# Kernel tuning notes

Measured on AMD Instinct MI355X. Metric: run time of the kernel, lower is better.

Reference implementation:

```python
import jax, jax.numpy as jnp
import numpy as np

MAX_CLUSTERS = 5
CLUSTER_SIZE_MAX = 3
K_HOP = 2
TAU = 1.0  # epoch=0 -> tau_init * decay^0 = 1.0
NEG = -1e9


def _logits(x, ctx, W1, b1, W2, b2):
    # x: [B,N,D], ctx: [B,H] -> logits [B,N] (selection_mlp, dropout=eval/identity)
    B, N, _ = x.shape
    h = jnp.concatenate([x, jnp.broadcast_to(ctx[:, None, :], (B, N, ctx.shape[-1]))], axis=-1)
    h = jax.nn.relu(h @ W1.T + b1)
    return (h @ W2.T + b2)[..., 0]


def _select(logits, cand, key):
    # Hard Gumbel-Softmax argmax over candidate nodes; zeros row if no candidates.
    any_c = cand.any(axis=-1, keepdims=True)
    ml = jnp.where(cand, logits, NEG)
    u = jax.random.uniform(key, logits.shape, dtype=logits.dtype)
    g = -jnp.log(-jnp.log(u + 1e-8) + 1e-8)
    idx = jnp.argmax((ml + g) / TAU, axis=-1)
    oh = jax.nn.one_hot(idx, logits.shape[-1], dtype=logits.dtype)
    return oh * any_c.astype(logits.dtype)


def _gru(seq, h0, Wih, Whh, bih, bhh):
    # torch nn.GRU single layer, batch_first; seq: [B,T,D], h0: [B,H] -> final hidden [B,H]
    def cell(h, xt):
        gi = xt @ Wih.T + bih
        gh = h @ Whh.T + bhh
        ir, iz, inn = jnp.split(gi, 3, axis=-1)
        hr, hz, hn = jnp.split(gh, 3, axis=-1)
        r = jax.nn.sigmoid(ir + hr)
        z = jax.nn.sigmoid(iz + hz)
        n = jnp.tanh(inn + r * hn)
        return (1.0 - z) * n + z * h, None
    h, _ = jax.lax.scan(cell, h0, jnp.swapaxes(seq, 0, 1))
    return h


def reference(x, adj, mask, W1, b1, W2, b2, Wc, bc, Wih, Whh, bih, bhh):
    B, N, D = x.shape
    key = jax.random.key(42)
    avail = mask.astype(bool)
    ctx = x.mean(axis=1) @ Wc.T + bc          # context_init  [B,H]
    h_gru = jnp.zeros_like(ctx)               # context_hidden
    assign = jnp.zeros((B, N, MAX_CLUSTERS), x.dtype)
    embs, hist = [], []
    for c in range(MAX_CLUSTERS):
        # logits are identical for every selection within this cluster (same x, same context)
        logits = _logits(x, ctx, W1, b1, W2, b2)  # [B,N]
        # seed selection (torch uses .item() -> selection is a constant index; no grad path)
        seed = jax.lax.stop_gradient(_select(logits, avail, jax.random.fold_in(key, 2 * c)))
        avail = avail & ~(seed > 0.5)
        # k-hop BFS from seed via adjacency matvecs
        reach = seed > 0.5
        cur = seed
        for _ in range(K_HOP):
            nb = jnp.einsum('bn,bnm->bm', cur, adj) > 0
            new = nb & ~reach
            reach = reach | nb
            cur = new.astype(x.dtype)
        member = seed
        for a in range(CLUSTER_SIZE_MAX - 1):
            cand = avail & reach
            sel = jax.lax.stop_gradient(_select(logits, cand, jax.random.fold_in(key, 2 * c + 1000 + a)))
            avail = avail & ~(sel > 0.5)
            member = member + sel
        assign = assign.at[:, :, c].set(member)
        cnt = member.sum(axis=-1, keepdims=True)
        emb = jnp.einsum('bn,bnd->bd', member, x) / jnp.maximum(cnt, 1.0)  # mean of member feats; 0 if empty
        embs.append(emb)
        hist.append(emb)
        # torch re-runs the GRU over the FULL cluster history each iteration, starting
        # from the previously updated hidden state (faithful to the original code)
        h_gru = _gru(jnp.stack(hist, axis=1), h_gru, Wih, Whh, bih, bhh)
        ctx = h_gru
    cluster_features = jnp.stack(embs, axis=1)               # [B,S,D]
    S = MAX_CLUSTERS
    cluster_adj = jnp.ones((B, S, S), x.dtype) - jnp.eye(S, dtype=x.dtype)[None]
    return cluster_features, cluster_adj, assign


def setup_inputs() -> dict:
    key = jax.random.key(0)
    ks = jax.random.split(key, 10)
    B, N, D, H = 16, 2048, 128, 64
    x = jax.random.normal(ks[0], (B, N, D), dtype=jnp.float32)
    # sparse symmetric binary adjacency, ~16 neighbors per node
    a = (jax.random.uniform(ks[1], (B, N, N)) < 0.004).astype(jnp.float32)
    adj = jnp.clip(a + jnp.swapaxes(a, 1, 2), 0.0, 1.0)
    adj = adj * (1.0 - jnp.eye(N, dtype=jnp.float32)[None])
    mask = jnp.ones((B, N), dtype=jnp.int32)
    s = 0.05
    return {
        'x': x, 'adj': adj, 'mask': mask,
        'W1': jax.random.normal(ks[2], (H, D + H)) * s, 'b1': jnp.zeros((H,)),
        'W2': jax.random.normal(ks[3], (1, H)) * s, 'b2': jnp.zeros((1,)),
        'Wc': jax.random.normal(ks[4], (H, D)) * s, 'bc': jnp.zeros((H,)),
        'Wih': jax.random.normal(ks[5], (3 * H, D)) * s,
        'Whh': jax.random.normal(ks[6], (3 * H, H)) * s,
        'bih': jnp.zeros((3 * H,)), 'bhh': jnp.zeros((3 * H,)),
    }
```

## Files before the change

### kernel.cpp

```cpp
#include <hip/hip_runtime.h>
#include <cfloat>
#include <cmath>

#define NB 2048
#define BB 16
#define DD 128
#define HH 64
#define MAXC 5
#define CSMAX 3
#define NT 1024

__device__ __forceinline__ unsigned rotl32(unsigned v, int d) {
  return (v << d) | (v >> (32 - d));
}

__device__ __forceinline__ void tf2x32(unsigned k0, unsigned k1, unsigned x0, unsigned x1,
                                       unsigned& o0, unsigned& o1) {
  unsigned ks2 = k0 ^ k1 ^ 0x1BD11BDAu;
  x0 += k0; x1 += k1;
#define RND(r) { x0 += x1; x1 = rotl32(x1, r); x1 ^= x0; }
  RND(13) RND(15) RND(26) RND(6)   x0 += k1;  x1 += ks2 + 1u;
  RND(17) RND(29) RND(16) RND(24)  x0 += ks2; x1 += k0 + 2u;
  RND(13) RND(15) RND(26) RND(6)   x0 += k0;  x1 += k1 + 3u;
  RND(17) RND(29) RND(16) RND(24)  x0 += k1;  x1 += ks2 + 4u;
  RND(13) RND(15) RND(26) RND(6)   x0 += ks2; x1 += k0 + 5u;
#undef RND
  o0 = x0; o1 = x1;
}

__device__ __forceinline__ float gumbel_for(unsigned k0, unsigned k1, unsigned idx) {
  unsigned o0, o1;
  tf2x32(k0, k1, 0u, idx, o0, o1);
  unsigned bits = o0 ^ o1;
  float u = __uint_as_float((bits >> 9) | 0x3f800000u) - 1.0f;
  float uu = u + 1e-8f;
  return -logf(-logf(uu) + 1e-8f);
}

__global__ __launch_bounds__(NT) void gvp_prep(
    const float* __restrict__ x, const float* __restrict__ W1,
    float* __restrict__ P, float* __restrict__ partial, float* __restrict__ gumb) {
  __shared__ __align__(16) float s_W1[HH][DD + 4];
  __shared__ float sp[8][DD];
  const int bid = blockIdx.x, tid = threadIdx.x;

  if (bid < 128) {
    for (int i = tid; i < HH * (DD / 4); i += NT) {
      int r = i >> 5, q = i & 31;
      *(float4*)&s_W1[r][q * 4] = *(const float4*)(W1 + (size_t)r * (DD + HH) + q * 4);
    }
    __syncthreads();
    const int jg = tid & 15, ng = tid >> 4;
    const int j0 = jg * 4;
    const size_t n0 = (size_t)bid * 256 + ng * 4;
    const float4* x4 = (const float4*)x;
    float acc[4][4];
#pragma unroll
    for (int i = 0; i < 4; i++)
#pragma unroll
      for (int q = 0; q < 4; q++) acc[i][q] = 0.f;
    for (int kq = 0; kq < 32; kq++) {
      float4 xv[4], wv[4];
#pragma unroll
      for (int i = 0; i < 4; i++) xv[i] = x4[(n0 + i) * 32 + kq];
#pragma unroll
      for (int q = 0; q < 4; q++) wv[q] = *(const float4*)&s_W1[j0 + q][kq * 4];
#pragma unroll
      for (int i = 0; i < 4; i++)
#pragma unroll
        for (int q = 0; q < 4; q++)
          acc[i][q] += xv[i].x * wv[q].x + xv[i].y * wv[q].y +
                       xv[i].z * wv[q].z + xv[i].w * wv[q].w;
    }
#pragma unroll
    for (int i = 0; i < 4; i++)
#pragma unroll
      for (int q = 0; q < 4; q++)
        P[(n0 + i) * HH + j0 + q] = acc[i][q];
  } else if (bid < 384) {
    const int bm = bid - 128;
    const int b = bm >> 4, chunk = bm & 15;
    const int d = tid & (DD - 1), part = tid >> 7;
    float acc = 0.f;
    const int base = chunk * 128 + part;
#pragma unroll
    for (int k = 0; k < 16; k++)
      acc += x[((size_t)b * NB + base + k * 8) * DD + d];
    sp[part][d] = acc;
    __syncthreads();
    if (tid < DD) {
      float m = 0.f;
#pragma unroll
      for (int p = 0; p < 8; p++) m += sp[p][tid];
      partial[((size_t)b * 16 + chunk) * DD + tid] = m;
    }
  } else {
    const int bg = bid - 384;
    const int base = (bg * NT + tid) * 4;
#pragma unroll
    for (int i = 0; i < 4; i++) {
      int idx = base + i;
      int sel = idx >> 15;
      int rem = idx & 32767;
      int c = sel / 3, s = sel - 3 * c;
      unsigned data = (s == 0) ? (unsigned)(2 * c) : (unsigned)(2 * c + 1000 + (s - 1));
      unsigned k0, k1;
      tf2x32(0u, 42u, 0u, data, k0, k1);
      gumb[idx] = gumbel_for(k0, k1, (unsigned)rem);
    }
  }
}

__global__ __launch_bounds__(NT, 4) void gvp_main(
    const float* __restrict__ x, const float* __restrict__ adj, const int* __restrict__ mask,
    const float* __restrict__ W1, const float* __restrict__ b1,
    const float* __restrict__ W2, const float* __restrict__ b2,
    const float* __restrict__ Wc, const float* __restrict__ bc,
    const float* __restrict__ Wih, const float* __restrict__ Whh,
    const float* __restrict__ bih, const float* __restrict__ bhh,
    const float* __restrict__ P, const float* __restrict__ partial,
    const float* __restrict__ gumb,
    float* __restrict__ out_feat, float* __restrict__ out_adjm, float* __restrict__ out_assign) {
  const int b = blockIdx.x;
  const int tid = threadIdx.x;

  __shared__ __align__(16) float s_logits[NB];
  __shared__ __align__(16) float s_gumb[2][NB];
  __shared__ unsigned char s_avail[NB], s_reach[NB], s_assignB[NB];
  __shared__ short s_list[128];
  __shared__ int s_cnt;
  __shared__ unsigned long long s_key[CSMAX];
  __shared__ __align__(16) float s_ctx[HH], s_q[HH];
  __shared__ __align__(16) float s_h[2][HH];
  __shared__ __align__(16) float s_hist[MAXC][DD];
  __shared__ __align__(16) float s_giAll[MAXC][3 * HH];
  __shared__ __align__(16) float s_Whh[3 * HH][HH + 4];
  __shared__ __align__(16) float s_W1c[HH][HH + 4];
  __shared__ __align__(16) float s_W2[HH];
  __shared__ float s_bhh[3 * HH], s_b1[HH];
  __shared__ __align__(16) float s_mean[DD];
  __shared__ float s_b2v;

  const size_t xb = (size_t)b * NB * DD;
  const float4* adj4 = (const float4*)(adj + (size_t)b * NB * NB);
  const float4* P4 = (const float4*)(P + (size_t)b * NB * HH);
  const int n0 = tid, n1 = tid + NT;

  auto scanReduce = [&](float bv, int bi, int slot) {
#pragma unroll
    for (int off = 32; off; off >>= 1) {
      float ov = __shfl_down(bv, off);
      int oi = __shfl_down(bi, off);
      if (ov > bv || (ov == bv && oi < bi)) { bv = ov; bi = oi; }
    }
    if ((tid & 63) == 0 && bi < NB) {
      unsigned u = __float_as_uint(bv);
      u = (u & 0x80000000u) ? ~u : (u | 0x80000000u);
      unsigned long long key = ((unsigned long long)u << 32) | (unsigned)(~bi);
      atomicMax(&s_key[slot], key);
    }
  };
  auto decodeIdx = [](unsigned long long k) -> int {
    return k ? (int)(unsigned)(~(unsigned)k) : -1;
  };

  float4 pP[16];
  {
    const float4* pr0 = P4 + (size_t)n0 * 16;
#pragma unroll
    for (int i = 0; i < 16; i++) pP[i] = pr0[i];
  }
  for (int i = tid; i < 3 * HH * (HH / 4); i += NT) {
    int r = i >> 4, q = i & 15;
    *(float4*)&s_Whh[r][q * 4] = *(const float4*)(Whh + (size_t)r * HH + q * 4);
  }
  {
    int r = tid >> 4, q = tid & 15;
    *(float4*)&s_W1c[r][q * 4] = *(const float4*)(W1 + (size_t)r * (DD + HH) + DD + q * 4);
  }
  if (tid < 3 * HH) s_bhh[tid] = bhh[tid];
  if (tid < HH) { s_W2[tid] = W2[tid]; s_b1[tid] = b1[tid]; s_h[0][tid] = 0.f; }
  if (tid == 0) s_b2v = b2[0];
#pragma unroll
  for (int r = 0; r < 2; r++) {
    int n = tid + r * NT;
    s_avail[n] = (mask[b * NB + n] != 0) ? 1 : 0;
    s_assignB[n] = 0;
  }
  if (tid < DD) {
    float m = 0.f;
#pragma unroll
    for (int k = 0; k < 16; k++) m += partial[((size_t)b * 16 + k) * DD + tid];
    s_mean[tid] = m * (1.0f / NB);
  }
  float4 gst;
  float g0a, g0b;
  {
    const float* g0p = gumb + ((size_t)0 * BB + b) * NB;
    g0a = g0p[n0]; g0b = g0p[n1];
    const float4* g12 = (const float4*)(gumb + ((size_t)(1 + (tid >> 9)) * BB + b) * NB);
    gst = g12[tid & 511];
  }
  __syncthreads();
  if (tid < 4 * HH) {
    int row = tid >> 2, g = tid & 3;
    const float4* wr = (const float4*)(Wc + (size_t)row * DD) + g * 8;
    const float4* m4 = (const float4*)s_mean + g * 8;
    float s = 0.f;
#pragma unroll
    for (int i = 0; i < 8; i++) {
      float4 w = wr[i], m = m4[i];
      s += w.x * m.x + w.y * m.y + w.z * m.z + w.w * m.w;
    }
    s += __shfl_xor(s, 1);
    s += __shfl_xor(s, 2);
    if (g == 0) s_ctx[row] = s + bc[row];
  }
  __syncthreads();

  int hp = 0;

  auto gruStep = [&](int t, int lo, int c) {
    int tt = tid - lo;
    if ((unsigned)tt < 256u) {
      int row = tt >> 2, g = tt & 3;
      const float4* h4 = (const float4*)s_h[hp] + g * 4;
      float4 hv[4];
#pragma unroll
      for (int i = 0; i < 4; i++) hv[i] = h4[i];
      const float4* wr = (const float4*)&s_Whh[row][0] + g * 4;
      const float4* wz = (const float4*)&s_Whh[HH + row][0] + g * 4;
      const float4* wn = (const float4*)&s_Whh[2 * HH + row][0] + g * 4;
      float sr = 0.f, sz = 0.f, sn = 0.f;
#pragma unroll
      for (int i = 0; i < 4; i++) {
        float4 a = wr[i], bz = wz[i], cn = wn[i], h = hv[i];
        sr += a.x * h.x + a.y * h.y + a.z * h.z + a.w * h.w;
        sz += bz.x * h.x + bz.y * h.y + bz.z * h.z + bz.w * h.w;
        sn += cn.x * h.x + cn.y * h.y + cn.z * h.z + cn.w * h.w;
      }
      sr += __shfl_xor(sr, 1); sr += __shfl_xor(sr, 2);
      sz += __shfl_xor(sz, 1); sz += __shfl_xor(sz, 2);
      sn += __shfl_xor(sn, 1); sn += __shfl_xor(sn, 2);
      if (g == 0) {
        float r = 1.f / (1.f + expf(-(s_giAll[t][row] + sr + s_bhh[row])));
        float z = 1.f / (1.f + expf(-(s_giAll[t][HH + row] + sz + s_bhh[HH + row])));
        float nn = tanhf(s_giAll[t][2 * HH + row] + r * (sn + s_bhh[2 * HH + row]));
        float hn = (1.f - z) * nn + z * s_h[hp][row];
        s_h[hp ^ 1][row] = hn;
        if (t == c) s_ctx[row] = hn;
      }
    }
  };

  for (int c = 0; c < MAXC; c++) {
    ((float4*)s_gumb)[tid] = gst;
    if (tid < 4 * HH) {
      int row = tid >> 2, g = tid & 3;
      const float4* wr = (const float4*)&s_W1c[row][0] + g * 4;
      const float4* c4 = (const float4*)s_ctx + g * 4;
      float s = 0.f;
#pragma unroll
      for (int i = 0; i < 4; i++) {
        float4 w = wr[i], cc = c4[i];
        s += w.x * cc.x + w.y * cc.y + w.z * cc.z + w.w * cc.w;
      }
      s += __shfl_xor(s, 1);
      s += __shfl_xor(s, 2);
      if (g == 0) s_q[row] = s + s_b1[row];
    }
    if (tid >= 512 && tid < 512 + CSMAX) s_key[tid - 512] = 0ull;
    if (tid == 768) s_cnt = 0;
    __syncthreads();

    {
      const float4* p1 = P4 + (size_t)n1 * 16;
      const float4* q4 = (const float4*)s_q;
      const float4* w4 = (const float4*)s_W2;
      float4 Pa[8];
#pragma unroll
      for (int i = 0; i < 8; i++) Pa[i] = p1[i];
      float l0 = s_b2v, l1 = s_b2v;
#pragma unroll
      for (int i = 0; i < 16; i++) {
        float4 p = pP[i], qv = q4[i], w = w4[i];
        l0 += w.x * fmaxf(p.x + qv.x, 0.f) + w.y * fmaxf(p.y + qv.y, 0.f) +
              w.z * fmaxf(p.z + qv.z, 0.f) + w.w * fmaxf(p.w + qv.w, 0.f);
      }
#pragma unroll
      for (int i = 0; i < 8; i++) {
        float4 p = Pa[i], qv = q4[i], w = w4[i];
        l1 += w.x * fmaxf(p.x + qv.x, 0.f) + w.y * fmaxf(p.y + qv.y, 0.f) +
              w.z * fmaxf(p.z + qv.z, 0.f) + w.w * fmaxf(p.w + qv.w, 0.f);
      }
#pragma unroll
      for (int i = 0; i < 8; i++) Pa[i] = p1[8 + i];
#pragma unroll
      for (int i = 0; i < 8; i++) {
        float4 p = Pa[i], qv = q4[8 + i], w = w4[8 + i];
        l1 += w.x * fmaxf(p.x + qv.x, 0.f) + w.y * fmaxf(p.y + qv.y, 0.f) +
              w.z * fmaxf(p.z + qv.z, 0.f) + w.w * fmaxf(p.w + qv.w, 0.f);
      }
      s_logits[n0] = l0;
      s_logits[n1] = l1;
      float bv = -FLT_MAX;
      int bi = NB;
      if (s_avail[n0]) { float y = l0 + g0a; if (y > bv) { bv = y; bi = n0; } }
      if (s_avail[n1]) { float y = l1 + g0b; if (y > bv || (y == bv && n1 < bi)) { bv = y; bi = n1; } }
      scanReduce(bv, bi, 0);
    }
    __syncthreads();

    const int seed = decodeIdx(s_key[0]);
    if (tid < 512) {
      if (seed >= 0) {
        float4 a = adj4[(size_t)seed * 512 + tid];
        int m = tid << 2;
        unsigned f0 = a.x > 0.f, f1 = a.y > 0.f, f2 = a.z > 0.f, f3 = a.w > 0.f;
        unsigned r = f0 | (f1 << 8) | (f2 << 16) | (f3 << 24);
        if ((seed >> 2) == tid) r |= 1u << ((seed & 3) * 8);
        ((unsigned*)s_reach)[tid] = r;
        if (f0 && m != seed)     { int p = atomicAdd(&s_cnt, 1); if (p < 128) s_list[p] = (short)m; }
        if (f1 && m + 1 != seed) { int p = atomicAdd(&s_cnt, 1); if (p < 128) s_list[p] = (short)(m + 1); }
        if (f2 && m + 2 != seed) { int p = atomicAdd(&s_cnt, 1); if (p < 128) s_list[p] = (short)(m + 2); }
        if (f3 && m + 3 != seed) { int p = atomicAdd(&s_cnt, 1); if (p < 128) s_list[p] = (short)(m + 3); }
      } else {
        ((unsigned*)s_reach)[tid] = 0u;
      }
    }
    __syncthreads();

    if (seed >= 0) {
      int cnt = min(s_cnt, 128);
      int m4 = tid & 511, rg = tid >> 9;
      bool a0 = false, a1 = false, a2 = false, a3 = false;
#pragma unroll
      for (int k = 0; k < 20; k++) {
        int li = rg + 2 * k;
        if (li < cnt) {
          int n = s_list[li];
          float4 a = adj4[(size_t)n * 512 + m4];
          a0 |= a.x > 0.f; a1 |= a.y > 0.f; a2 |= a.z > 0.f; a3 |= a.w > 0.f;
        }
      }
      for (int li = rg + 40; li < cnt; li += 2) {
        int n = s_list[li];
        float4 a = adj4[(size_t)n * 512 + m4];
        a0 |= a.x > 0.f; a1 |= a.y > 0.f; a2 |= a.z > 0.f; a3 |= a.w > 0.f;
      }
      int m = m4 << 2;
      if (a0) s_reach[m] = 1;
      if (a1) s_reach[m + 1] = 1;
      if (a2) s_reach[m + 2] = 1;
      if (a3) s_reach[m + 3] = 1;
    }
    __syncthreads();

    {
      float bv = -FLT_MAX;
      int bi = NB;
#pragma unroll
      for (int r = 0; r < 2; r++) {
        int n = tid + r * NT;
        if (s_avail[n] && s_reach[n] && n != seed) {
          float y = s_logits[n] + s_gumb[0][n];
          if (y > bv || (y == bv && n < bi)) { bv = y; bi = n; }
        }
      }
      scanReduce(bv, bi, 1);
    }
    __syncthreads();

    const int w1i = decodeIdx(s_key[1]);
    {
      float bv = -FLT_MAX;
      int bi = NB;
#pragma unroll
      for (int r = 0; r < 2; r++) {
        int n = tid + r * NT;
        if (s_avail[n] && s_reach[n] && n != seed && n != w1i) {
          float y = s_logits[n] + s_gumb[1][n];
          if (y > bv || (y == bv && n < bi)) { bv = y; bi = n; }
        }
      }
      scanReduce(bv, bi, 2);
    }
    __syncthreads();

    const int w2i = decodeIdx(s_key[2]);
    if (c + 1 < MAXC) {
      const float* g0p = gumb + ((size_t)((c + 1) * 3) * BB + b) * NB;
      g0a = g0p[n0]; g0b = g0p[n1];
      const float4* g12 =
          (const float4*)(gumb + ((size_t)((c + 1) * 3 + 1 + (tid >> 9)) * BB + b) * NB);
      gst = g12[tid & 511];
    }
    {
      int mc = (seed >= 0) + (w1i >= 0) + (w2i >= 0);
      if (tid < DD) {
        float acc = 0.f;
        if (seed >= 0) acc += x[xb + (size_t)seed * DD + tid];
        if (w1i >= 0) acc += x[xb + (size_t)w1i * DD + tid];
        if (w2i >= 0) acc += x[xb + (size_t)w2i * DD + tid];
        float e = acc / fmaxf((float)mc, 1.0f);
        s_hist[c][tid] = e;
        out_feat[((size_t)b * MAXC + c) * DD + tid] = e;
      } else if (tid >= 512 && tid < 512 + CSMAX) {
        int idx = (tid == 512) ? seed : (tid == 513 ? w1i : w2i);
        if (idx >= 0) { s_avail[idx] = 0; s_assignB[idx] |= (unsigned char)(1 << c); }
      }
      if (c >= 1) gruStep(0, 256, c);
    }
    __syncthreads();
    if (c >= 1) hp ^= 1;

    if (tid < 4 * 3 * HH) {
      int row = tid >> 2, g = tid & 3;
      const float4* wr = (const float4*)(Wih + (size_t)row * DD) + g * 8;
      const float4* h4 = (const float4*)s_hist[c] + g * 8;
      float s = 0.f;
#pragma unroll
      for (int i = 0; i < 8; i++) {
        float4 w = wr[i], hh = h4[i];
        s += w.x * hh.x + w.y * hh.y + w.z * hh.z + w.w * hh.w;
      }
      s += __shfl_xor(s, 1);
      s += __shfl_xor(s, 2);
      if (g == 0) s_giAll[c][row] = s + bih[row];
    }
    if (c >= 2) gruStep(1, 768, c);
    __syncthreads();
    if (c >= 2) hp ^= 1;

    int t0 = (c == 0) ? 0 : (c == 1) ? 1 : 2;
    for (int t = t0; t <= c; t++) {
      gruStep(t, 0, c);
      hp ^= 1;
      __syncthreads();
    }
  }

#pragma unroll
  for (int r = 0; r < 2; r++) {
    int n = tid + r * NT;
    unsigned bits = s_assignB[n];
    size_t base = ((size_t)(b * NB + n)) * MAXC;
#pragma unroll
    for (int cc = 0; cc < MAXC; cc++)
      out_assign[base + cc] = (float)((bits >> cc) & 1u);
  }
  for (int i = tid; i < MAXC * MAXC; i += NT)
    out_adjm[(size_t)b * MAXC * MAXC + i] = ((i / MAXC) == (i % MAXC)) ? 0.f : 1.f;
}

extern "C" void kernel_launch(void* const* d_in, const int* in_sizes, int n_in,
                              void* d_out, int out_size, void* d_ws, size_t ws_size,
                              hipStream_t stream) {
  const float* x   = (const float*)d_in[0];
  const float* adj = (const float*)d_in[1];
  const int*   mask= (const int*)d_in[2];
  const float* W1  = (const float*)d_in[3];
  const float* b1  = (const float*)d_in[4];
  const float* W2  = (const float*)d_in[5];
  const float* b2  = (const float*)d_in[6];
  const float* Wc  = (const float*)d_in[7];
  const float* bc  = (const float*)d_in[8];
  const float* Wih = (const float*)d_in[9];
  const float* Whh = (const float*)d_in[10];
  const float* bih = (const float*)d_in[11];
  const float* bhh = (const float*)d_in[12];

  float* ws = (float*)d_ws;
  float* P       = ws;
  float* partial = P + (size_t)BB * NB * HH;
  float* gumb    = partial + (size_t)BB * 16 * DD;

  float* out = (float*)d_out;
  float* out_feat = out;
  float* out_adjm = out + (size_t)BB * MAXC * DD;
  float* out_assign = out_adjm + (size_t)BB * MAXC * MAXC;

  hipLaunchKernelGGL(gvp_prep, dim3(504), dim3(NT), 0, stream, x, W1, P, partial, gumb);
  hipLaunchKernelGGL(gvp_main, dim3(BB), dim3(NT), 0, stream,
                     x, adj, mask, W1, b1, W2, b2, Wc, bc, Wih, Whh, bih, bhh, P, partial, gumb,
                     out_feat, out_adjm, out_assign);
}
```

Before: 209.3 us.

## Keep P rows and Wih slices in registers and use lighter LDS-only barriers

Loads both P rows (n0 and n1) and each thread's Wih slice into named registers once, before the cluster loop, so they are not re-read from global memory every cluster. Replaces __syncthreads with a barrier that waits only on LDS counters, so outstanding global loads are not drained at every phase. Pins waves_per_eu to 4 to fix the register budget. The extra live registers risk spilling, and the weaker barrier relies on no global-memory ordering being needed between phases.

Result: faster. 201.9 us (-3.5%).

```diff
diff --git a/kernel.cpp b/kernel.cpp
--- a/kernel.cpp
+++ b/kernel.cpp
@@ -37,6 +37,16 @@
   return -logf(-logf(uu) + 1e-8f);
 }
 
+__device__ __forceinline__ void phase_barrier() {
+  asm volatile("s_waitcnt lgkmcnt(0)" ::: "memory");
+  __builtin_amdgcn_s_barrier();
+  asm volatile("" ::: "memory");
+}
+
+#define REP16(M) M(0) M(1) M(2) M(3) M(4) M(5) M(6) M(7) \
+                 M(8) M(9) M(10) M(11) M(12) M(13) M(14) M(15)
+#define REP8(M) M(0) M(1) M(2) M(3) M(4) M(5) M(6) M(7)
+
 __global__ __launch_bounds__(NT) void gvp_prep(
     const float* __restrict__ x, const float* __restrict__ W1,
     float* __restrict__ P, float* __restrict__ partial, float* __restrict__ gumb) {
@@ -111,7 +121,8 @@
   }
 }
 
-__global__ __launch_bounds__(NT, 4) void gvp_main(
+__global__ __launch_bounds__(NT, 4) __attribute__((amdgpu_waves_per_eu(4, 4)))
+void gvp_main(
     const float* __restrict__ x, const float* __restrict__ adj, const int* __restrict__ mask,
     const float* __restrict__ W1, const float* __restrict__ b1,
     const float* __restrict__ W2, const float* __restrict__ b2,
@@ -164,34 +175,20 @@
     return k ? (int)(unsigned)(~(unsigned)k) : -1;
   };
 
-  float4 pP[16];
+#define DECLP(i) float4 pA##i, pB##i;
+  REP16(DECLP)
+#define DECLW(i) float4 wv##i;
+  REP8(DECLW)
   {
-    const float4* pr0 = P4 + (size_t)n0 * 16;
-#pragma unroll
-    for (int i = 0; i < 16; i++) pP[i] = pr0[i];
-  }
-  for (int i = tid; i < 3 * HH * (HH / 4); i += NT) {
-    int r = i >> 4, q = i & 15;
-    *(float4*)&s_Whh[r][q * 4] = *(const float4*)(Whh + (size_t)r * HH + q * 4);
-  }
-  {
-    int r = tid >> 4, q = tid & 15;
-    *(float4*)&s_W1c[r][q * 4] = *(const float4*)(W1 + (size_t)r * (DD + HH) + DD + q * 4);
-  }
-  if (tid < 3 * HH) s_bhh[tid] = bhh[tid];
-  if (tid < HH) { s_W2[tid] = W2[tid]; s_b1[tid] = b1[tid]; s_h[0][tid] = 0.f; }
-  if (tid == 0) s_b2v = b2[0];
-#pragma unroll
-  for (int r = 0; r < 2; r++) {
-    int n = tid + r * NT;
-    s_avail[n] = (mask[b * NB + n] != 0) ? 1 : 0;
-    s_assignB[n] = 0;
-  }
-  if (tid < DD) {
-    float m = 0.f;
-#pragma unroll
-    for (int k = 0; k < 16; k++) m += partial[((size_t)b * 16 + k) * DD + tid];
-    s_mean[tid] = m * (1.0f / NB);
+    const float4* p0r = P4 + (size_t)n0 * 16;
+    const float4* p1r = P4 + (size_t)n1 * 16;
+#define LOADP(i) pA##i = p0r[i]; pB##i = p1r[i];
+    REP16(LOADP)
+  }
+  if (tid < 4 * 3 * HH) {
+    const float4* wr = (const float4*)Wih + ((size_t)(tid >> 2) * 32 + (tid & 3) * 8);
+#define LOADW(i) wv##i = wr[i];
+    REP8(LOADW)
   }
   float4 gst;
   float g0a, g0b;
@@ -201,7 +198,31 @@
     const float4* g12 = (const float4*)(gumb + ((size_t)(1 + (tid >> 9)) * BB + b) * NB);
     gst = g12[tid & 511];
   }
-  __syncthreads();
+
+  for (int i = tid; i < 3 * HH * (HH / 4); i += NT) {
+    int r = i >> 4, q = i & 15;
+    *(float4*)&s_Whh[r][q * 4] = *(const float4*)(Whh + (size_t)r * HH + q * 4);
+  }
+  {
+    int r = tid >> 4, q = tid & 15;
+    *(float4*)&s_W1c[r][q * 4] = *(const float4*)(W1 + (size_t)r * (DD + HH) + DD + q * 4);
+  }
+  if (tid < 3 * HH) s_bhh[tid] = bhh[tid];
+  if (tid < HH) { s_W2[tid] = W2[tid]; s_b1[tid] = b1[tid]; s_h[0][tid] = 0.f; }
+  if (tid == 0) s_b2v = b2[0];
+#pragma unroll
+  for (int r = 0; r < 2; r++) {
+    int n = tid + r * NT;
+    s_avail[n] = (mask[b * NB + n] != 0) ? 1 : 0;
+    s_assignB[n] = 0;
+  }
+  if (tid < DD) {
+    float m = 0.f;
+#pragma unroll
+    for (int k = 0; k < 16; k++) m += partial[((size_t)b * 16 + k) * DD + tid];
+    s_mean[tid] = m * (1.0f / NB);
+  }
+  phase_barrier();
   if (tid < 4 * HH) {
     int row = tid >> 2, g = tid & 3;
     const float4* wr = (const float4*)(Wc + (size_t)row * DD) + g * 8;
@@ -216,7 +237,7 @@
     s += __shfl_xor(s, 2);
     if (g == 0) s_ctx[row] = s + bc[row];
   }
-  __syncthreads();
+  phase_barrier();
 
   int hp = 0;
 
@@ -271,36 +292,18 @@
     }
     if (tid >= 512 && tid < 512 + CSMAX) s_key[tid - 512] = 0ull;
     if (tid == 768) s_cnt = 0;
-    __syncthreads();
+    phase_barrier();
 
     {
-      const float4* p1 = P4 + (size_t)n1 * 16;
       const float4* q4 = (const float4*)s_q;
       const float4* w4 = (const float4*)s_W2;
-      float4 Pa[8];
-#pragma unroll
-      for (int i = 0; i < 8; i++) Pa[i] = p1[i];
       float l0 = s_b2v, l1 = s_b2v;
-#pragma unroll
-      for (int i = 0; i < 16; i++) {
-        float4 p = pP[i], qv = q4[i], w = w4[i];
-        l0 += w.x * fmaxf(p.x + qv.x, 0.f) + w.y * fmaxf(p.y + qv.y, 0.f) +
-              w.z * fmaxf(p.z + qv.z, 0.f) + w.w * fmaxf(p.w + qv.w, 0.f);
-      }
-#pragma unroll
-      for (int i = 0; i < 8; i++) {
-        float4 p = Pa[i], qv = q4[i], w = w4[i];
-        l1 += w.x * fmaxf(p.x + qv.x, 0.f) + w.y * fmaxf(p.y + qv.y, 0.f) +
-              w.z * fmaxf(p.z + qv.z, 0.f) + w.w * fmaxf(p.w + qv.w, 0.f);
-      }
-#pragma unroll
-      for (int i = 0; i < 8; i++) Pa[i] = p1[8 + i];
-#pragma unroll
-      for (int i = 0; i < 8; i++) {
-        float4 p = Pa[i], qv = q4[8 + i], w = w4[8 + i];
-        l1 += w.x * fmaxf(p.x + qv.x, 0.f) + w.y * fmaxf(p.y + qv.y, 0.f) +
-              w.z * fmaxf(p.z + qv.z, 0.f) + w.w * fmaxf(p.w + qv.w, 0.f);
-      }
+#define ACC(i) { float4 qv = q4[i], w = w4[i]; \
+      l0 += w.x * fmaxf(pA##i.x + qv.x, 0.f) + w.y * fmaxf(pA##i.y + qv.y, 0.f) + \
+            w.z * fmaxf(pA##i.z + qv.z, 0.f) + w.w * fmaxf(pA##i.w + qv.w, 0.f); \
+      l1 += w.x * fmaxf(pB##i.x + qv.x, 0.f) + w.y * fmaxf(pB##i.y + qv.y, 0.f) + \
+            w.z * fmaxf(pB##i.z + qv.z, 0.f) + w.w * fmaxf(pB##i.w + qv.w, 0.f); }
+      REP16(ACC)
       s_logits[n0] = l0;
       s_logits[n1] = l1;
       float bv = -FLT_MAX;
@@ -309,7 +312,7 @@
       if (s_avail[n1]) { float y = l1 + g0b; if (y > bv || (y == bv && n1 < bi)) { bv = y; bi = n1; } }
       scanReduce(bv, bi, 0);
     }
-    __syncthreads();
+    phase_barrier();
 
     const int seed = decodeIdx(s_key[0]);
     if (tid < 512) {
@@ -328,7 +331,7 @@
         ((unsigned*)s_reach)[tid] = 0u;
       }
     }
-    __syncthreads();
+    phase_barrier();
 
     if (seed >= 0) {
       int cnt = min(s_cnt, 128);
@@ -354,7 +357,7 @@
       if (a2) s_reach[m + 2] = 1;
       if (a3) s_reach[m + 3] = 1;
     }
-    __syncthreads();
+    phase_barrier();
 
     {
       float bv = -FLT_MAX;
@@ -369,7 +372,7 @@
       }
       scanReduce(bv, bi, 1);
     }
-    __syncthreads();
+    phase_barrier();
 
     const int w1i = decodeIdx(s_key[1]);
     {
@@ -385,7 +388,7 @@
       }
       scanReduce(bv, bi, 2);
     }
-    __syncthreads();
+    phase_barrier();
 
     const int w2i = decodeIdx(s_key[2]);
     if (c + 1 < MAXC) {
@@ -411,32 +414,29 @@
       }
       if (c >= 1) gruStep(0, 256, c);
     }
-    __syncthreads();
+    phase_barrier();
     if (c >= 1) hp ^= 1;
 
     if (tid < 4 * 3 * HH) {
-      int row = tid >> 2, g = tid & 3;
-      const float4* wr = (const float4*)(Wih + (size_t)row * DD) + g * 8;
+      int g = tid & 3;
       const float4* h4 = (const float4*)s_hist[c] + g * 8;
       float s = 0.f;
-#pragma unroll
-      for (int i = 0; i < 8; i++) {
-        float4 w = wr[i], hh = h4[i];
-        s += w.x * hh.x + w.y * hh.y + w.z * hh.z + w.w * hh.w;
-      }
+#define GACC(i) { float4 hh = h4[i]; s += wv##i.x * hh.x + wv##i.y * hh.y + \
+                  wv##i.z * hh.z + wv##i.w * hh.w; }
+      REP8(GACC)
       s += __shfl_xor(s, 1);
       s += __shfl_xor(s, 2);
-      if (g == 0) s_giAll[c][row] = s + bih[row];
+      if (g == 0) s_giAll[c][tid >> 2] = s + bih[tid >> 2];
     }
     if (c >= 2) gruStep(1, 768, c);
-    __syncthreads();
+    phase_barrier();
     if (c >= 2) hp ^= 1;
 
     int t0 = (c == 0) ? 0 : (c == 1) ? 1 : 2;
     for (int t = t0; t <= c; t++) {
       gruStep(t, 0, c);
       hp ^= 1;
-      __syncthreads();
+      phase_barrier();
     }
   }
 
```
